# Performance work log

Hardware: AMD Instinct MI355X
Metric: run time of the kernel (lower is better)

The kernel has to match this reference:

```python
import jax, jax.numpy as jnp
import numpy as np

N_ENT, N_USR, N_ITEM, N_REL, N_CLS, N_FAC, D = 100000, 4096, 8192, 32, 3, 8, 128
N_EDGES, NNZ = 800000, 204800


def setup_inputs() -> dict:
    key = jax.random.key(0)
    ks = jax.random.split(key, 15)
    return {
        "entity_emb": jax.random.normal(ks[0], (N_ENT, D), jnp.float32),
        "item_emb": jax.random.normal(ks[1], (N_ITEM, D), jnp.float32),
        "user_emb": jax.random.normal(ks[2], (N_USR, D), jnp.float32),
        "latent_emb": jax.random.normal(ks[3], (N_FAC, D), jnp.float32),
        "relation_emb": jax.random.normal(ks[4], (N_REL, D), jnp.float32),
        "edge_index": jax.random.randint(ks[5], (2, N_EDGES), 0, N_ENT, jnp.int32),
        "edge_type": jax.random.randint(ks[6], (N_EDGES,), 0, N_REL, jnp.int32),
        "edge_imp": jax.random.uniform(ks[7], (N_EDGES,), jnp.float32),
        "inter_rows": jax.random.randint(ks[8], (NNZ,), 0, N_USR, jnp.int32),
        "inter_cols": jax.random.randint(ks[9], (NNZ,), 0, N_ENT, jnp.int32),
        "inter_vals": jax.random.uniform(ks[10], (NNZ,), jnp.float32),
        "disen_weight_att": jax.random.normal(ks[11], (N_FAC, N_REL), jnp.float32),
        "ent_rel_w": jax.random.normal(ks[12], (N_REL, D), jnp.float32),
        "usr_cls_w": jax.random.normal(ks[13], (N_CLS, D), jnp.float32),
        "inter_cls_mat": jax.random.normal(ks[14], (N_CLS, N_USR, N_ITEM), jnp.float32),
    }


def reference(entity_emb, item_emb, user_emb, latent_emb, relation_emb,
              edge_index, edge_type, edge_imp, inter_rows, inter_cols,
              inter_vals, disen_weight_att, ent_rel_w, usr_cls_w, inter_cls_mat):
    n_entities = entity_emb.shape[0]
    n_users = user_emb.shape[0]
    head, tail = edge_index[0], edge_index[1]

    # --- entity aggregation, e_mode='att_imp' ---
    # per-entity attention over relations: [n_ent, n_rel]
    ent_rel_att = jax.nn.softmax(entity_emb @ relation_emb.T, axis=1)
    mess_att = ent_rel_att[head, edge_type][:, None]              # [E,1]
    message_score = relation_emb[edge_type] * mess_att * edge_imp[:, None]  # [E,D]
    message = entity_emb[tail] * message_score                    # [E,D]
    entity_agg = jax.ops.segment_sum(message, head, num_segments=n_entities)

    # --- user aggregation, u_mode='inter_cls' ---
    # sparse interact_mat @ entity_emb via COO gather + segment_sum
    user_agg = jax.ops.segment_sum(entity_emb[inter_cols] * inter_vals[:, None],
                                   inter_rows, num_segments=n_users)
    user_cls_att = jax.nn.softmax(user_emb @ usr_cls_w.T, axis=1)  # [U,C]
    item_emb_2 = item_emb * relation_emb.sum(axis=0, keepdims=True)  # [I,D]
    # stack_c(inter_cls_mat[c] @ item_emb_2).transpose(0,1) -> [U,C,D]
    disen_weight = jnp.einsum('cui,id->ucd', inter_cls_mat, item_emb_2)
    user_agg = user_agg + (disen_weight * user_cls_att[:, :, None]).sum(axis=1)

    return entity_agg, user_agg
```

## Files before the change

### kernel.cpp

```cpp
#include <hip/hip_runtime.h>

#define N_ENT   100000
#define N_USR   4096
#define N_ITEM  8192
#define N_REL   32
#define N_CLS   3
#define DD      128
#define N_EDGES 800000
#define NNZ     204800

#define CAP_E   64
#define CAP_U   128

typedef __attribute__((ext_vector_type(8))) short short8;
typedef __attribute__((ext_vector_type(4))) float f32x4;

static __device__ __forceinline__ unsigned short f2bf(float x) {
    unsigned int u = __builtin_bit_cast(unsigned int, x);
    u = (u + 0x7fffu + ((u >> 16) & 1u)) >> 16;
    return (unsigned short)u;
}
static __device__ __forceinline__ float bflo(unsigned int v) {
    return __uint_as_float(v << 16);
}
static __device__ __forceinline__ float bfhi(unsigned int v) {
    return __uint_as_float(v & 0xffff0000u);
}

#define ZB  ((N_ENT + N_USR + 255) / 256)

__global__ __launch_bounds__(256) void k_prep_light(const float* __restrict__ rel,
                                                    int* __restrict__ cnt,
                                                    const float* __restrict__ item,
                                                    unsigned short* __restrict__ Bt,
                                                    const float* __restrict__ usr,
                                                    const float* __restrict__ w,
                                                    float* __restrict__ uatt) {
    __shared__ float smem[32 * 33 + 32];
    int bx = blockIdx.x;

    if (bx < ZB) {
        int i = bx * 256 + threadIdx.x;
        if (i < N_ENT + N_USR) cnt[i] = 0;
        return;
    }
    bx -= ZB;

    if (bx < 1024) {
        float (*tile)[33] = (float(*)[33])smem;
        float* ssum = smem + 32 * 33;
        const int b2 = bx & 255, by = bx >> 8;
        const int tx = threadIdx.x & 31, ty = threadIdx.x >> 5;
        const int i0 = b2 * 32, d0 = by * 32;
        if (threadIdx.x < 32) {
            float s = 0.f;
            for (int r = 0; r < N_REL; ++r) s += rel[r * DD + d0 + threadIdx.x];
            ssum[threadIdx.x] = s;
        }
#pragma unroll
        for (int rr = 0; rr < 4; ++rr)
            tile[ty + 8 * rr][tx] = item[(size_t)(i0 + ty + 8 * rr) * DD + d0 + tx];
        __syncthreads();
#pragma unroll
        for (int rr = 0; rr < 4; ++rr) {
            int d = d0 + ty + 8 * rr;
            Bt[(size_t)d * N_ITEM + i0 + tx] = f2bf(tile[tx][ty + 8 * rr] * ssum[ty + 8 * rr]);
        }
        return;
    }
    bx -= 1024;

    {
        for (int i = threadIdx.x; i < N_CLS * DD; i += 256) smem[i] = w[i];
        __syncthreads();
        int u = bx * 256 + threadIdx.x;
        const float4* row = (const float4*)(usr + (size_t)u * DD);
        float acc[3] = {0.f, 0.f, 0.f};
        for (int dq = 0; dq < DD / 4; ++dq) {
            float4 v = row[dq];
#pragma unroll
            for (int c = 0; c < 3; ++c) {
                float4 ww = *(const float4*)&smem[c * DD + dq * 4];
                acc[c] += v.x * ww.x + v.y * ww.y + v.z * ww.z + v.w * ww.w;
            }
        }
        float m = fmaxf(acc[0], fmaxf(acc[1], acc[2]));
        float s = 0.f;
#pragma unroll
        for (int c = 0; c < 3; ++c) { acc[c] = __expf(acc[c] - m); s += acc[c]; }
        float inv = 1.f / s;
#pragma unroll
        for (int c = 0; c < 3; ++c) uatt[u * 3 + c] = acc[c] * inv;
    }
}

#define EAB ((N_ENT + 255) / 256)
#define SCAT_BLOCKS ((N_EDGES + 255) / 256)

__global__ __launch_bounds__(256) void k_att_scatter(const float* __restrict__ ent,
                                                     const float* __restrict__ rel,
                                                     float* __restrict__ att,
                                                     unsigned short* __restrict__ entbf,
                                                     unsigned short* __restrict__ relbf,
                                                     const int* __restrict__ eidx,
                                                     const int* __restrict__ etyp,
                                                     const float* __restrict__ eimp,
                                                     const int* __restrict__ irow,
                                                     const int* __restrict__ icol,
                                                     const float* __restrict__ ival,
                                                     int* __restrict__ cnt,
                                                     int2* __restrict__ pack_e,
                                                     int2* __restrict__ pack_u) {
    __shared__ float smemf[N_REL * DD];

    if (blockIdx.x < EAB) {
        int bx = blockIdx.x;
        for (int i = threadIdx.x; i < N_REL * DD; i += 256) smemf[i] = rel[i];
        __syncthreads();
        if (bx == 0) {
            for (int i = threadIdx.x; i < N_REL * DD; i += 256)
                relbf[i] = f2bf(smemf[i]);
        }
        int e = bx * 256 + threadIdx.x;
        if (e >= N_ENT) return;
        const float4* row = (const float4*)(ent + (size_t)e * DD);
        unsigned short* brow = entbf + (size_t)e * DD;
        float acc[N_REL];
#pragma unroll
        for (int r = 0; r < N_REL; ++r) acc[r] = 0.f;
        for (int dq = 0; dq < DD / 4; ++dq) {
            float4 v = row[dq];
            ushort4 bv;
            bv.x = f2bf(v.x); bv.y = f2bf(v.y); bv.z = f2bf(v.z); bv.w = f2bf(v.w);
            *(ushort4*)(brow + dq * 4) = bv;
#pragma unroll
            for (int r = 0; r < N_REL; ++r) {
                float4 ww = *(const float4*)&smemf[r * DD + dq * 4];
                acc[r] += v.x * ww.x + v.y * ww.y + v.z * ww.z + v.w * ww.w;
            }
        }
        float m = acc[0];
#pragma unroll
        for (int r = 1; r < N_REL; ++r) m = fmaxf(m, acc[r]);
        float s = 0.f;
#pragma unroll
        for (int r = 0; r < N_REL; ++r) { acc[r] = __expf(acc[r] - m); s += acc[r]; }
        float inv = 1.f / s;
        float* o = att + (size_t)e * N_REL;
#pragma unroll
        for (int r = 0; r < N_REL; ++r) o[r] = acc[r] * inv;
    } else {
        int i = (blockIdx.x - EAB) * 256 + threadIdx.x;
        if (i < N_EDGES) {
            int h = eidx[i], tl = eidx[N_EDGES + i], r = etyp[i];
            int p = atomicAdd(&cnt[h], 1);
            if (p < CAP_E) {
                int2 pk;
                pk.x = tl | (r << 24);
                pk.y = __float_as_int(eimp[i]);
                pack_e[(size_t)h * CAP_E + p] = pk;
            }
        }
        if (i < NNZ) {
            int u = irow[i];
            int p = atomicAdd(&cnt[N_ENT + u], 1);
            if (p < CAP_U) {
                int2 pk;
                pk.x = icol[i];
                pk.y = __float_as_int(ival[i]);
                pack_u[(size_t)u * CAP_U + p] = pk;
            }
        }
    }
}

#define BM 64
#define BK 32
#define SPLITK 16
#define KCH (N_ITEM / SPLITK)
#define PLANE ((long long)N_USR * N_ITEM)
#define GEMM_BLOCKS ((N_USR / BM) * SPLITK)

__global__ __launch_bounds__(256) void k_disen_gemm(const float* __restrict__ icm,
                                                    const unsigned short* __restrict__ Bt,
                                                    const float* __restrict__ uatt,
                                                    float* __restrict__ part) {
    __shared__ unsigned short sA[BM][40];
    __shared__ unsigned short sB[DD][40];

    const int t  = threadIdx.x;
    const int m0 = blockIdx.x * BM;
    const long long k0b = (long long)blockIdx.y * KCH;

    const int ua = t >> 3;
    const int qa = t & 7;
    const float a00 = uatt[(m0 + ua) * 3 + 0];
    const float a01 = uatt[(m0 + ua) * 3 + 1];
    const float a02 = uatt[(m0 + ua) * 3 + 2];
    const float a10 = uatt[(m0 + ua + 32) * 3 + 0];
    const float a11 = uatt[(m0 + ua + 32) * 3 + 1];
    const float a12 = uatt[(m0 + ua + 32) * 3 + 2];

    const int db = t >> 2;
    const int qb = t & 3;

    const int lane = t & 63;
    const int wv = t >> 6;
    const int wm = wv >> 1, wn = wv & 1;
    const int la = lane & 15, lb = lane >> 4;

    f32x4 acc[2][4];
#pragma unroll
    for (int mi = 0; mi < 2; ++mi)
#pragma unroll
        for (int ni = 0; ni < 4; ++ni) {
            f32x4 z = {0.f, 0.f, 0.f, 0.f};
            acc[mi][ni] = z;
        }

    float4 rA0[3], rA1[3];
    short8 rB0, rB1;
    {
        const long long base0 = (long long)(m0 + ua) * N_ITEM + k0b + qa * 4;
        rA0[0] = *(const float4*)(icm + base0);
        rA0[1] = *(const float4*)(icm + base0 + PLANE);
        rA0[2] = *(const float4*)(icm + base0 + 2 * PLANE);
        const long long base1 = base0 + 32ll * N_ITEM;
        rA1[0] = *(const float4*)(icm + base1);
        rA1[1] = *(const float4*)(icm + base1 + PLANE);
        rA1[2] = *(const float4*)(icm + base1 + 2 * PLANE);
        const unsigned short* g0 = Bt + (long long)db * N_ITEM + k0b + qb * 8;
        rB0 = *(const short8*)g0;
        rB1 = *(const short8*)(g0 + 64ll * N_ITEM);
    }

    for (int kk = 0; kk < KCH; kk += BK) {
        __syncthreads();
        {
            ushort4 p;
            p.x = f2bf(a00 * rA0[0].x + a01 * rA0[1].x + a02 * rA0[2].x);
            p.y = f2bf(a00 * rA0[0].y + a01 * rA0[1].y + a02 * rA0[2].y);
            p.z = f2bf(a00 * rA0[0].z + a01 * rA0[1].z + a02 * rA0[2].z);
            p.w = f2bf(a00 * rA0[0].w + a01 * rA0[1].w + a02 * rA0[2].w);
            *(ushort4*)(&sA[ua][0] + qa * 4) = p;
            p.x = f2bf(a10 * rA1[0].x + a11 * rA1[1].x + a12 * rA1[2].x);
            p.y = f2bf(a10 * rA1[0].y + a11 * rA1[1].y + a12 * rA1[2].y);
            p.z = f2bf(a10 * rA1[0].z + a11 * rA1[1].z + a12 * rA1[2].z);
            p.w = f2bf(a10 * rA1[0].w + a11 * rA1[1].w + a12 * rA1[2].w);
            *(ushort4*)(&sA[ua + 32][0] + qa * 4) = p;
            *(short8*)(&sB[db][0] + qb * 8) = rB0;
            *(short8*)(&sB[db + 64][0] + qb * 8) = rB1;
        }
        __syncthreads();

        if (kk + BK < KCH) {
            const long long k0 = k0b + kk + BK;
            const long long base0 = (long long)(m0 + ua) * N_ITEM + k0 + qa * 4;
            rA0[0] = *(const float4*)(icm + base0);
            rA0[1] = *(const float4*)(icm + base0 + PLANE);
            rA0[2] = *(const float4*)(icm + base0 + 2 * PLANE);
            const long long base1 = base0 + 32ll * N_ITEM;
            rA1[0] = *(const float4*)(icm + base1);
            rA1[1] = *(const float4*)(icm + base1 + PLANE);
            rA1[2] = *(const float4*)(icm + base1 + 2 * PLANE);
            const unsigned short* g0 = Bt + (long long)db * N_ITEM + k0 + qb * 8;
            rB0 = *(const short8*)g0;
            rB1 = *(const short8*)(g0 + 64ll * N_ITEM);
        }

        short8 af[2], bfr[4];
#pragma unroll
        for (int mi = 0; mi < 2; ++mi)
            af[mi] = *(const short8*)(&sA[wm * 32 + mi * 16 + la][0] + lb * 8);
#pragma unroll
        for (int ni = 0; ni < 4; ++ni)
            bfr[ni] = *(const short8*)(&sB[wn * 64 + ni * 16 + la][0] + lb * 8);
#pragma unroll
        for (int mi = 0; mi < 2; ++mi)
#pragma unroll
            for (int ni = 0; ni < 4; ++ni)
                acc[mi][ni] = __builtin_amdgcn_mfma_f32_16x16x32_bf16(
                    af[mi], bfr[ni], acc[mi][ni], 0, 0, 0);
    }

    float* pbase = part + (size_t)blockIdx.y * ((size_t)N_USR * DD);
#pragma unroll
    for (int mi = 0; mi < 2; ++mi)
#pragma unroll
        for (int ni = 0; ni < 4; ++ni)
#pragma unroll
            for (int r = 0; r < 4; ++r) {
                int row = m0 + wm * 32 + mi * 16 + lb * 4 + r;
                int col = wn * 64 + ni * 16 + la;
                pbase[(size_t)row * DD + col] = acc[mi][ni][r];
            }
}

#define EDGE_BLOCKS (N_ENT / 16)
#define USER_BLOCKS (N_USR / 4)

__global__ __launch_bounds__(256) void k_node3(const unsigned short* __restrict__ entbf,
                                               const unsigned short* __restrict__ relbf,
                                               const float* __restrict__ att,
                                               const int2* __restrict__ pack_e,
                                               const int2* __restrict__ pack_u,
                                               const int* __restrict__ cnt,
                                               const float* __restrict__ part,
                                               float* __restrict__ out_ent,
                                               float* __restrict__ out_usr) {
    const int lane = threadIdx.x & 63;

    if (blockIdx.x < EDGE_BLOCKS) {
        const int wid = blockIdx.x * 4 + (threadIdx.x >> 6);
        const int l15 = lane & 15;
        const int grp = lane >> 4;
#pragma unroll 1
        for (int hh = 0; hh < 4; ++hh) {
            const int h = wid * 4 + hh;
            const int n = min(cnt[h], CAP_E);
            const float attv = att[(size_t)h * N_REL + (lane & 31)];
            const int2* seg = pack_e + (size_t)h * CAP_E;
            float acc[8];
#pragma unroll
            for (int e = 0; e < 8; ++e) acc[e] = 0.f;
            for (int j = 0; j < n; j += 8) {
                const int e0 = j + grp, e1 = j + 4 + grp;
                int2 p0 = seg[min(e0, n - 1)];
                int2 p1 = seg[min(e1, n - 1)];
                const int r0 = ((unsigned)p0.x) >> 24;
                const int r1 = ((unsigned)p1.x) >> 24;
                float s0 = __shfl(attv, r0, 64) * __int_as_float(p0.y);
                float s1 = __shfl(attv, r1, 64) * __int_as_float(p1.y);
                s0 = (e0 < n) ? s0 : 0.f;
                s1 = (e1 < n) ? s1 : 0.f;
                uint4 b0 = ((const uint4*)(entbf + (size_t)(p0.x & 0xFFFFFF) * DD))[l15];
                uint4 b1 = ((const uint4*)(entbf + (size_t)(p1.x & 0xFFFFFF) * DD))[l15];
                uint4 v0 = ((const uint4*)(relbf + (size_t)r0 * DD))[l15];
                uint4 v1 = ((const uint4*)(relbf + (size_t)r1 * DD))[l15];
                const unsigned* bp0 = (const unsigned*)&b0;
                const unsigned* bp1 = (const unsigned*)&b1;
                const unsigned* vp0 = (const unsigned*)&v0;
                const unsigned* vp1 = (const unsigned*)&v1;
#pragma unroll
                for (int q = 0; q < 4; ++q) {
                    acc[2 * q]     = fmaf(bflo(bp0[q]) * bflo(vp0[q]), s0, acc[2 * q]);
                    acc[2 * q + 1] = fmaf(bfhi(bp0[q]) * bfhi(vp0[q]), s0, acc[2 * q + 1]);
                    acc[2 * q]     = fmaf(bflo(bp1[q]) * bflo(vp1[q]), s1, acc[2 * q]);
                    acc[2 * q + 1] = fmaf(bfhi(bp1[q]) * bfhi(vp1[q]), s1, acc[2 * q + 1]);
                }
            }
#pragma unroll
            for (int e = 0; e < 8; ++e) {
                acc[e] += __shfl_xor(acc[e], 16, 64);
                acc[e] += __shfl_xor(acc[e], 32, 64);
            }
            if (lane < 16) {
                float4 o0 = {acc[0], acc[1], acc[2], acc[3]};
                float4 o1 = {acc[4], acc[5], acc[6], acc[7]};
                float4* dst = (float4*)(out_ent + (size_t)h * DD) + l15 * 2;
                dst[0] = o0;
                dst[1] = o1;
            }
        }
    } else {
        const int u = (blockIdx.x - EDGE_BLOCKS) * 4 + (threadIdx.x >> 6);
        const int n = min(cnt[N_ENT + u], CAP_U);
        const int2* seg = pack_u + (size_t)u * CAP_U;
        float ax = 0.f, ay = 0.f;
        for (int j = 0; j < n; j += 8) {
            int2 pk[8];
#pragma unroll
            for (int k = 0; k < 8; ++k) pk[k] = seg[min(j + k, n - 1)];
            unsigned int bv[8];
            float sc[8];
#pragma unroll
            for (int k = 0; k < 8; ++k) {
                sc[k] = (j + k < n) ? __int_as_float(pk[k].y) : 0.f;
                bv[k] = ((const unsigned int*)(entbf + (size_t)pk[k].x * DD))[lane];
            }
#pragma unroll
            for (int k = 0; k < 8; ++k) {
                ax = fmaf(bflo(bv[k]), sc[k], ax);
                ay = fmaf(bfhi(bv[k]), sc[k], ay);
            }
        }
#pragma unroll
        for (int k = 0; k < SPLITK; ++k) {
            float2 p = ((const float2*)(part + (size_t)k * N_USR * DD + (size_t)u * DD))[lane];
            ax += p.x;
            ay += p.y;
        }
        float2 o; o.x = ax; o.y = ay;
        ((float2*)(out_usr + (size_t)u * DD))[lane] = o;
    }
}

static constexpr size_t algn(size_t x) { return (x + 255) & ~(size_t)255; }

extern "C" void kernel_launch(void* const* d_in, const int* in_sizes, int n_in,
                              void* d_out, int out_size, void* d_ws, size_t ws_size,
                              hipStream_t stream) {
    const float* ent  = (const float*)d_in[0];
    const float* item = (const float*)d_in[1];
    const float* usr  = (const float*)d_in[2];
    const float* rel  = (const float*)d_in[4];
    const int*   eidx = (const int*)d_in[5];
    const int*   etyp = (const int*)d_in[6];
    const float* eimp = (const float*)d_in[7];
    const int*   irow = (const int*)d_in[8];
    const int*   icol = (const int*)d_in[9];
    const float* ival = (const float*)d_in[10];
    const float* uclw = (const float*)d_in[13];
    const float* icm  = (const float*)d_in[14];

    float* out_ent = (float*)d_out;
    float* out_usr = out_ent + (size_t)N_ENT * DD;

    char* w = (char*)d_ws;
    size_t o = 0;
    float* ws_att  = (float*)(w + o);  o = algn(o + (size_t)N_ENT * N_REL * 4);
    float* ws_uatt = (float*)(w + o);  o = algn(o + (size_t)N_USR * N_CLS * 4);
    unsigned short* ws_Bt    = (unsigned short*)(w + o); o = algn(o + (size_t)DD * N_ITEM * 2);
    unsigned short* ws_entbf = (unsigned short*)(w + o); o = algn(o + (size_t)N_ENT * DD * 2);
    unsigned short* ws_relbf = (unsigned short*)(w + o); o = algn(o + (size_t)N_REL * DD * 2);
    int*  ws_cnt   = (int*)(w + o);  o = algn(o + (size_t)(N_ENT + N_USR) * 4);
    int2* pack_e   = (int2*)(w + o); o = algn(o + (size_t)N_ENT * CAP_E * 8);
    int2* pack_u   = (int2*)(w + o); o = algn(o + (size_t)N_USR * CAP_U * 8);
    float* part    = (float*)(w + o); o = algn(o + (size_t)SPLITK * N_USR * DD * 4);

    (void)in_sizes; (void)n_in; (void)ws_size; (void)out_size;

    k_prep_light<<<ZB + 1024 + 16, 256, 0, stream>>>(rel, ws_cnt, item, ws_Bt,
                                                     usr, uclw, ws_uatt);
    k_att_scatter<<<EAB + SCAT_BLOCKS, 256, 0, stream>>>(ent, rel, ws_att, ws_entbf,
                                                         ws_relbf, eidx, etyp, eimp,
                                                         irow, icol, ival, ws_cnt,
                                                         pack_e, pack_u);
    k_disen_gemm<<<dim3(N_USR / BM, SPLITK), 256, 0, stream>>>(icm, ws_Bt, ws_uatt, part);
    k_node3<<<EDGE_BLOCKS + USER_BLOCKS, 256, 0, stream>>>(ws_entbf, ws_relbf, ws_att,
                                                           pack_e, pack_u, ws_cnt, part,
                                                           out_ent, out_usr);
}
```

Baseline: 312.5 us.

## Double-buffer LDS and prefetch two K-steps ahead in disen GEMM

Restructures the split-K GEMM main loop to use two LDS buffers and two register staging sets, issuing global loads two steps ahead. One barrier per step is removed, and more memory latency is hidden behind the MFMA work. The cost is doubled LDS use and more registers for staging, which may lower occupancy.

```diff
diff --git a/kernel.cpp b/kernel.cpp
--- a/kernel.cpp
+++ b/kernel.cpp
@@ -178,15 +178,61 @@
 #define BK 32
 #define SPLITK 16
 #define KCH (N_ITEM / SPLITK)
+#define NSTEP (KCH / BK)
 #define PLANE ((long long)N_USR * N_ITEM)
-#define GEMM_BLOCKS ((N_USR / BM) * SPLITK)
+
+#define ISSUE(rA_, rB_, step) do {                                            \
+    const long long k0_ = k0b + (long long)(step) * BK;                       \
+    const long long b0_ = (long long)(m0 + ua) * N_ITEM + k0_ + qa * 4;       \
+    rA_[0] = *(const float4*)(icm + b0_);                                     \
+    rA_[1] = *(const float4*)(icm + b0_ + PLANE);                             \
+    rA_[2] = *(const float4*)(icm + b0_ + 2 * PLANE);                         \
+    const long long b1_ = b0_ + 32ll * N_ITEM;                                \
+    rA_[3] = *(const float4*)(icm + b1_);                                     \
+    rA_[4] = *(const float4*)(icm + b1_ + PLANE);                             \
+    rA_[5] = *(const float4*)(icm + b1_ + 2 * PLANE);                         \
+    const unsigned short* g0_ = Bt + (long long)db * N_ITEM + k0_ + qb * 8;   \
+    rB_[0] = *(const short8*)g0_;                                             \
+    rB_[1] = *(const short8*)(g0_ + 64ll * N_ITEM);                           \
+} while (0)
+
+#define GBODY(rA_, rB_, BUF, step) do {                                       \
+    ushort4 p_;                                                               \
+    p_.x = f2bf(a00 * rA_[0].x + a01 * rA_[1].x + a02 * rA_[2].x);            \
+    p_.y = f2bf(a00 * rA_[0].y + a01 * rA_[1].y + a02 * rA_[2].y);            \
+    p_.z = f2bf(a00 * rA_[0].z + a01 * rA_[1].z + a02 * rA_[2].z);            \
+    p_.w = f2bf(a00 * rA_[0].w + a01 * rA_[1].w + a02 * rA_[2].w);            \
+    *(ushort4*)(&sA[BUF][ua][0] + qa * 4) = p_;                               \
+    p_.x = f2bf(a10 * rA_[3].x + a11 * rA_[4].x + a12 * rA_[5].x);            \
+    p_.y = f2bf(a10 * rA_[3].y + a11 * rA_[4].y + a12 * rA_[5].y);            \
+    p_.z = f2bf(a10 * rA_[3].z + a11 * rA_[4].z + a12 * rA_[5].z);            \
+    p_.w = f2bf(a10 * rA_[3].w + a11 * rA_[4].w + a12 * rA_[5].w);            \
+    *(ushort4*)(&sA[BUF][ua + 32][0] + qa * 4) = p_;                          \
+    *(short8*)(&sB[BUF][db][0] + qb * 8) = rB_[0];                            \
+    *(short8*)(&sB[BUF][db + 64][0] + qb * 8) = rB_[1];                       \
+    __syncthreads();                                                          \
+    if ((step) + 2 < NSTEP) ISSUE(rA_, rB_, (step) + 2);                      \
+    short8 af_[2], bf_[4];                                                    \
+    _Pragma("unroll")                                                         \
+    for (int mi = 0; mi < 2; ++mi)                                            \
+        af_[mi] = *(const short8*)(&sA[BUF][wm * 32 + mi * 16 + la][0] + lb * 8); \
+    _Pragma("unroll")                                                         \
+    for (int ni = 0; ni < 4; ++ni)                                            \
+        bf_[ni] = *(const short8*)(&sB[BUF][wn * 64 + ni * 16 + la][0] + lb * 8); \
+    _Pragma("unroll")                                                         \
+    for (int mi = 0; mi < 2; ++mi)                                            \
+        _Pragma("unroll")                                                     \
+        for (int ni = 0; ni < 4; ++ni)                                        \
+            acc[mi][ni] = __builtin_amdgcn_mfma_f32_16x16x32_bf16(            \
+                af_[mi], bf_[ni], acc[mi][ni], 0, 0, 0);                      \
+} while (0)
 
 __global__ __launch_bounds__(256) void k_disen_gemm(const float* __restrict__ icm,
                                                     const unsigned short* __restrict__ Bt,
                                                     const float* __restrict__ uatt,
                                                     float* __restrict__ part) {
-    __shared__ unsigned short sA[BM][40];
-    __shared__ unsigned short sB[DD][40];
+    __shared__ unsigned short sA[2][BM][40];
+    __shared__ unsigned short sB[2][DD][40];
 
     const int t  = threadIdx.x;
     const int m0 = blockIdx.x * BM;
@@ -218,69 +264,16 @@
             acc[mi][ni] = z;
         }
 
-    float4 rA0[3], rA1[3];
-    short8 rB0, rB1;
-    {
-        const long long base0 = (long long)(m0 + ua) * N_ITEM + k0b + qa * 4;
-        rA0[0] = *(const float4*)(icm + base0);
-        rA0[1] = *(const float4*)(icm + base0 + PLANE);
-        rA0[2] = *(const float4*)(icm + base0 + 2 * PLANE);
-        const long long base1 = base0 + 32ll * N_ITEM;
-        rA1[0] = *(const float4*)(icm + base1);
-        rA1[1] = *(const float4*)(icm + base1 + PLANE);
-        rA1[2] = *(const float4*)(icm + base1 + 2 * PLANE);
-        const unsigned short* g0 = Bt + (long long)db * N_ITEM + k0b + qb * 8;
-        rB0 = *(const short8*)g0;
-        rB1 = *(const short8*)(g0 + 64ll * N_ITEM);
-    }
-
-    for (int kk = 0; kk < KCH; kk += BK) {
-        __syncthreads();
-        {
-            ushort4 p;
-            p.x = f2bf(a00 * rA0[0].x + a01 * rA0[1].x + a02 * rA0[2].x);
-            p.y = f2bf(a00 * rA0[0].y + a01 * rA0[1].y + a02 * rA0[2].y);
-            p.z = f2bf(a00 * rA0[0].z + a01 * rA0[1].z + a02 * rA0[2].z);
-            p.w = f2bf(a00 * rA0[0].w + a01 * rA0[1].w + a02 * rA0[2].w);
-            *(ushort4*)(&sA[ua][0] + qa * 4) = p;
-            p.x = f2bf(a10 * rA1[0].x + a11 * rA1[1].x + a12 * rA1[2].x);
-            p.y = f2bf(a10 * rA1[0].y + a11 * rA1[1].y + a12 * rA1[2].y);
-            p.z = f2bf(a10 * rA1[0].z + a11 * rA1[1].z + a12 * rA1[2].z);
-            p.w = f2bf(a10 * rA1[0].w + a11 * rA1[1].w + a12 * rA1[2].w);
-            *(ushort4*)(&sA[ua + 32][0] + qa * 4) = p;
-            *(short8*)(&sB[db][0] + qb * 8) = rB0;
-            *(short8*)(&sB[db + 64][0] + qb * 8) = rB1;
-        }
-        __syncthreads();
-
-        if (kk + BK < KCH) {
-            const long long k0 = k0b + kk + BK;
-            const long long base0 = (long long)(m0 + ua) * N_ITEM + k0 + qa * 4;
-            rA0[0] = *(const float4*)(icm + base0);
-            rA0[1] = *(const float4*)(icm + base0 + PLANE);
-            rA0[2] = *(const float4*)(icm + base0 + 2 * PLANE);
-            const long long base1 = base0 + 32ll * N_ITEM;
-            rA1[0] = *(const float4*)(icm + base1);
-            rA1[1] = *(const float4*)(icm + base1 + PLANE);
-            rA1[2] = *(const float4*)(icm + base1 + 2 * PLANE);
-            const unsigned short* g0 = Bt + (long long)db * N_ITEM + k0 + qb * 8;
-            rB0 = *(const short8*)g0;
-            rB1 = *(const short8*)(g0 + 64ll * N_ITEM);
-        }
-
-        short8 af[2], bfr[4];
-#pragma unroll
-        for (int mi = 0; mi < 2; ++mi)
-            af[mi] = *(const short8*)(&sA[wm * 32 + mi * 16 + la][0] + lb * 8);
-#pragma unroll
-        for (int ni = 0; ni < 4; ++ni)
-            bfr[ni] = *(const short8*)(&sB[wn * 64 + ni * 16 + la][0] + lb * 8);
-#pragma unroll
-        for (int mi = 0; mi < 2; ++mi)
-#pragma unroll
-            for (int ni = 0; ni < 4; ++ni)
-                acc[mi][ni] = __builtin_amdgcn_mfma_f32_16x16x32_bf16(
-                    af[mi], bfr[ni], acc[mi][ni], 0, 0, 0);
+    float4 rAa[6], rAb[6];
+    short8 rBa[2], rBb[2];
+
+    ISSUE(rAa, rBa, 0);
+    ISSUE(rAb, rBb, 1);
+
+#pragma unroll 1
+    for (int s = 0; s < NSTEP; s += 2) {
+        GBODY(rAa, rBa, 0, s);
+        GBODY(rAb, rBb, 1, s + 1);
     }
 
     float* pbase = part + (size_t)blockIdx.y * ((size_t)N_USR * DD);
```

After: 316.0 us. No clear change (+1.1%).

## Precompute class-weighted bf16 interaction matrix before GEMM, simplify GEMM A loads

Applied to the files above, without the earlier changes.

Moves the attention-weighted reduction of the three inter_cls_mat planes into a separate streaming pass inside the attention/scatter kernel, writing a bf16 A matrix to workspace. The GEMM then loads compact bf16 A tiles instead of three fp32 planes plus conversion arithmetic per step. This lets the large read overlap with other prep work and lightens the GEMM inner loop, at the cost of an extra intermediate write and read-back and more workspace.

```diff
diff --git a/kernel.cpp b/kernel.cpp
--- a/kernel.cpp
+++ b/kernel.cpp
@@ -13,6 +13,7 @@
 #define CAP_U   128
 
 typedef __attribute__((ext_vector_type(8))) short short8;
+typedef __attribute__((ext_vector_type(4))) short short4v;
 typedef __attribute__((ext_vector_type(4))) float f32x4;
 
 static __device__ __forceinline__ unsigned short f2bf(float x) {
@@ -94,27 +95,57 @@
     }
 }
 
+#define PLANE  ((long long)N_USR * N_ITEM)
+#define PLANE4 (PLANE / 4)
+#define CB_BLOCKS ((int)(PLANE / 4096))
 #define EAB ((N_ENT + 255) / 256)
 #define SCAT_BLOCKS ((N_EDGES + 255) / 256)
 
-__global__ __launch_bounds__(256) void k_att_scatter(const float* __restrict__ ent,
-                                                     const float* __restrict__ rel,
-                                                     float* __restrict__ att,
-                                                     unsigned short* __restrict__ entbf,
-                                                     unsigned short* __restrict__ relbf,
-                                                     const int* __restrict__ eidx,
-                                                     const int* __restrict__ etyp,
-                                                     const float* __restrict__ eimp,
-                                                     const int* __restrict__ irow,
-                                                     const int* __restrict__ icol,
-                                                     const float* __restrict__ ival,
-                                                     int* __restrict__ cnt,
-                                                     int2* __restrict__ pack_e,
-                                                     int2* __restrict__ pack_u) {
+__global__ __launch_bounds__(256) void k_node2(const float* __restrict__ icm,
+                                               const float* __restrict__ uatt,
+                                               unsigned short* __restrict__ Abf,
+                                               const float* __restrict__ ent,
+                                               const float* __restrict__ rel,
+                                               float* __restrict__ att,
+                                               unsigned short* __restrict__ entbf,
+                                               unsigned short* __restrict__ relbf,
+                                               const int* __restrict__ eidx,
+                                               const int* __restrict__ etyp,
+                                               const float* __restrict__ eimp,
+                                               const int* __restrict__ irow,
+                                               const int* __restrict__ icol,
+                                               const float* __restrict__ ival,
+                                               int* __restrict__ cnt,
+                                               int2* __restrict__ pack_e,
+                                               int2* __restrict__ pack_u) {
     __shared__ float smemf[N_REL * DD];
 
-    if (blockIdx.x < EAB) {
-        int bx = blockIdx.x;
+    if (blockIdx.x < CB_BLOCKS) {
+        const int bid = blockIdx.x;
+        const int u = bid >> 1;
+        const float a0 = uatt[u * 3 + 0];
+        const float a1 = uatt[u * 3 + 1];
+        const float a2 = uatt[u * 3 + 2];
+        const float4* icm4 = (const float4*)icm;
+        const long long base4 = (long long)bid * 1024 + threadIdx.x;
+#pragma unroll
+        for (int j = 0; j < 4; ++j) {
+            long long idx4 = base4 + j * 256;
+            float4 f0 = icm4[idx4];
+            float4 f1 = icm4[idx4 + PLANE4];
+            float4 f2 = icm4[idx4 + 2 * PLANE4];
+            ushort4 o;
+            o.x = f2bf(a0 * f0.x + a1 * f1.x + a2 * f2.x);
+            o.y = f2bf(a0 * f0.y + a1 * f1.y + a2 * f2.y);
+            o.z = f2bf(a0 * f0.z + a1 * f1.z + a2 * f2.z);
+            o.w = f2bf(a0 * f0.w + a1 * f1.w + a2 * f2.w);
+            ((ushort4*)Abf)[idx4] = o;
+        }
+        return;
+    }
+
+    if (blockIdx.x < CB_BLOCKS + EAB) {
+        int bx = blockIdx.x - CB_BLOCKS;
         for (int i = threadIdx.x; i < N_REL * DD; i += 256) smemf[i] = rel[i];
         __syncthreads();
         if (bx == 0) {
@@ -149,8 +180,11 @@
         float* o = att + (size_t)e * N_REL;
 #pragma unroll
         for (int r = 0; r < N_REL; ++r) o[r] = acc[r] * inv;
-    } else {
-        int i = (blockIdx.x - EAB) * 256 + threadIdx.x;
+        return;
+    }
+
+    {
+        int i = (blockIdx.x - CB_BLOCKS - EAB) * 256 + threadIdx.x;
         if (i < N_EDGES) {
             int h = eidx[i], tl = eidx[N_EDGES + i], r = etyp[i];
             int p = atomicAdd(&cnt[h], 1);
@@ -178,13 +212,11 @@
 #define BK 32
 #define SPLITK 16
 #define KCH (N_ITEM / SPLITK)
-#define PLANE ((long long)N_USR * N_ITEM)
-#define GEMM_BLOCKS ((N_USR / BM) * SPLITK)
-
-__global__ __launch_bounds__(256) void k_disen_gemm(const float* __restrict__ icm,
-                                                    const unsigned short* __restrict__ Bt,
-                                                    const float* __restrict__ uatt,
-                                                    float* __restrict__ part) {
+#define NSTEP (KCH / BK)
+
+__global__ __launch_bounds__(256) void k_gemm2(const unsigned short* __restrict__ Abf,
+                                               const unsigned short* __restrict__ Bt,
+                                               float* __restrict__ part) {
     __shared__ unsigned short sA[BM][40];
     __shared__ unsigned short sB[DD][40];
 
@@ -194,13 +226,6 @@
 
     const int ua = t >> 3;
     const int qa = t & 7;
-    const float a00 = uatt[(m0 + ua) * 3 + 0];
-    const float a01 = uatt[(m0 + ua) * 3 + 1];
-    const float a02 = uatt[(m0 + ua) * 3 + 2];
-    const float a10 = uatt[(m0 + ua + 32) * 3 + 0];
-    const float a11 = uatt[(m0 + ua + 32) * 3 + 1];
-    const float a12 = uatt[(m0 + ua + 32) * 3 + 2];
-
     const int db = t >> 2;
     const int qb = t & 3;
 
@@ -218,55 +243,28 @@
             acc[mi][ni] = z;
         }
 
-    float4 rA0[3], rA1[3];
+    short4v rA0, rA1;
     short8 rB0, rB1;
-    {
-        const long long base0 = (long long)(m0 + ua) * N_ITEM + k0b + qa * 4;
-        rA0[0] = *(const float4*)(icm + base0);
-        rA0[1] = *(const float4*)(icm + base0 + PLANE);
-        rA0[2] = *(const float4*)(icm + base0 + 2 * PLANE);
-        const long long base1 = base0 + 32ll * N_ITEM;
-        rA1[0] = *(const float4*)(icm + base1);
-        rA1[1] = *(const float4*)(icm + base1 + PLANE);
-        rA1[2] = *(const float4*)(icm + base1 + 2 * PLANE);
-        const unsigned short* g0 = Bt + (long long)db * N_ITEM + k0b + qb * 8;
-        rB0 = *(const short8*)g0;
-        rB1 = *(const short8*)(g0 + 64ll * N_ITEM);
-    }
-
-    for (int kk = 0; kk < KCH; kk += BK) {
+
+#define GISSUE(step) do {                                                     \
+    const long long k0_ = k0b + (long long)(step) * BK;                       \
+    rA0 = *(const short4v*)(Abf + (size_t)(m0 + ua) * N_ITEM + k0_ + qa * 4); \
+    rA1 = *(const short4v*)(Abf + (size_t)(m0 + ua + 32) * N_ITEM + k0_ + qa * 4); \
+    rB0 = *(const short8*)(Bt + (size_t)db * N_ITEM + k0_ + qb * 8);          \
+    rB1 = *(const short8*)(Bt + (size_t)(db + 64) * N_ITEM + k0_ + qb * 8);   \
+} while (0)
+
+    GISSUE(0);
+
+#pragma unroll 1
+    for (int s = 0; s < NSTEP; ++s) {
         __syncthreads();
-        {
-            ushort4 p;
-            p.x = f2bf(a00 * rA0[0].x + a01 * rA0[1].x + a02 * rA0[2].x);
-            p.y = f2bf(a00 * rA0[0].y + a01 * rA0[1].y + a02 * rA0[2].y);
-            p.z = f2bf(a00 * rA0[0].z + a01 * rA0[1].z + a02 * rA0[2].z);
-            p.w = f2bf(a00 * rA0[0].w + a01 * rA0[1].w + a02 * rA0[2].w);
-            *(ushort4*)(&sA[ua][0] + qa * 4) = p;
-            p.x = f2bf(a10 * rA1[0].x + a11 * rA1[1].x + a12 * rA1[2].x);
-            p.y = f2bf(a10 * rA1[0].y + a11 * rA1[1].y + a12 * rA1[2].y);
-            p.z = f2bf(a10 * rA1[0].z + a11 * rA1[1].z + a12 * rA1[2].z);
-            p.w = f2bf(a10 * rA1[0].w + a11 * rA1[1].w + a12 * rA1[2].w);
-            *(ushort4*)(&sA[ua + 32][0] + qa * 4) = p;
-            *(short8*)(&sB[db][0] + qb * 8) = rB0;
-            *(short8*)(&sB[db + 64][0] + qb * 8) = rB1;
-        }
+        *(short4v*)(&sA[ua][qa * 4]) = rA0;
+        *(short4v*)(&sA[ua + 32][qa * 4]) = rA1;
+        *(short8*)(&sB[db][qb * 8]) = rB0;
+        *(short8*)(&sB[db + 64][qb * 8]) = rB1;
         __syncthreads();
-
-        if (kk + BK < KCH) {
-            const long long k0 = k0b + kk + BK;
-            const long long base0 = (long long)(m0 + ua) * N_ITEM + k0 + qa * 4;
-            rA0[0] = *(const float4*)(icm + base0);
-            rA0[1] = *(const float4*)(icm + base0 + PLANE);
-            rA0[2] = *(const float4*)(icm + base0 + 2 * PLANE);
-            const long long base1 = base0 + 32ll * N_ITEM;
-            rA1[0] = *(const float4*)(icm + base1);
-            rA1[1] = *(const float4*)(icm + base1 + PLANE);
-            rA1[2] = *(const float4*)(icm + base1 + 2 * PLANE);
-            const unsigned short* g0 = Bt + (long long)db * N_ITEM + k0 + qb * 8;
-            rB0 = *(const short8*)g0;
-            rB1 = *(const short8*)(g0 + 64ll * N_ITEM);
-        }
+        if (s + 1 < NSTEP) GISSUE(s + 1);
 
         short8 af[2], bfr[4];
 #pragma unroll
@@ -282,6 +280,7 @@
                 acc[mi][ni] = __builtin_amdgcn_mfma_f32_16x16x32_bf16(
                     af[mi], bfr[ni], acc[mi][ni], 0, 0, 0);
     }
+#undef GISSUE
 
     float* pbase = part + (size_t)blockIdx.y * ((size_t)N_USR * DD);
 #pragma unroll
@@ -423,6 +422,7 @@
     unsigned short* ws_Bt    = (unsigned short*)(w + o); o = algn(o + (size_t)DD * N_ITEM * 2);
     unsigned short* ws_entbf = (unsigned short*)(w + o); o = algn(o + (size_t)N_ENT * DD * 2);
     unsigned short* ws_relbf = (unsigned short*)(w + o); o = algn(o + (size_t)N_REL * DD * 2);
+    unsigned short* ws_Abf   = (unsigned short*)(w + o); o = algn(o + (size_t)N_USR * N_ITEM * 2);
     int*  ws_cnt   = (int*)(w + o);  o = algn(o + (size_t)(N_ENT + N_USR) * 4);
     int2* pack_e   = (int2*)(w + o); o = algn(o + (size_t)N_ENT * CAP_E * 8);
     int2* pack_u   = (int2*)(w + o); o = algn(o + (size_t)N_USR * CAP_U * 8);
@@ -432,11 +432,10 @@
 
     k_prep_light<<<ZB + 1024 + 16, 256, 0, stream>>>(rel, ws_cnt, item, ws_Bt,
                                                      usr, uclw, ws_uatt);
-    k_att_scatter<<<EAB + SCAT_BLOCKS, 256, 0, stream>>>(ent, rel, ws_att, ws_entbf,
-                                                         ws_relbf, eidx, etyp, eimp,
-                                                         irow, icol, ival, ws_cnt,
-                                                         pack_e, pack_u);
-    k_disen_gemm<<<dim3(N_USR / BM, SPLITK), 256, 0, stream>>>(icm, ws_Bt, ws_uatt, part);
+    k_node2<<<CB_BLOCKS + EAB + SCAT_BLOCKS, 256, 0, stream>>>(
+        icm, ws_uatt, ws_Abf, ent, rel, ws_att, ws_entbf, ws_relbf,
+        eidx, etyp, eimp, irow, icol, ival, ws_cnt, pack_e, pack_u);
+    k_gemm2<<<dim3(N_USR / BM, SPLITK), 256, 0, stream>>>(ws_Abf, ws_Bt, part);
     k_node3<<<EDGE_BLOCKS + USER_BLOCKS, 256, 0, stream>>>(ws_entbf, ws_relbf, ws_att,
                                                            pack_e, pack_u, ws_cnt, part,
                                                            out_ent, out_usr);
```

Result: faster. 299.3 us (-4.2%).
